# Performance work log

Measured on AMD Instinct MI355X. Metric: run time of the kernel, lower is better.

The kernel has to match this reference:

```python
import jax, jax.numpy as jnp
import numpy as np

B, M, N = 32, 512, 512
XD = YD = 512   # x_size, y_size
S = 512         # shared_size
H = 512         # hidden_size
MAXD = 11       # max relative distance


def _lin(k, i, o):
    lim = float(np.sqrt(6.0 / (i + o)))  # xavier_uniform, gain=1
    return jax.random.uniform(k, (i, o), jnp.float32, -lim, lim)


def setup_inputs() -> dict:
    key = jax.random.key(0)
    ks = jax.random.split(key, 16)
    inp = {
        'prem': jax.random.normal(ks[0], (B, M, YD), jnp.float32),
        'hypo': jax.random.normal(ks[1], (B, N, XD), jnp.float32),
        'prem_mask': jnp.ones((B, M), dtype=bool),
        'hypo_mask': jnp.ones((B, N), dtype=bool),
        # projections
        'Wpx': _lin(ks[2], XD, S), 'bpx': jnp.zeros((S,), jnp.float32),
        'Wpy': _lin(ks[3], YD, S), 'bpy': jnp.zeros((S,), jnp.float32),
        # relative-distance bias embedding (2*max_dist+1, squeezed to scalar)
        'dist_embed': jax.random.normal(ks[4], (2 * MAXD + 1,), jnp.float32),
        # self-attention DeepDot MLP: S -> H -> H
        'Ws1': _lin(ks[5], S, H), 'bs1': jnp.zeros((H,), jnp.float32),
        'Ws2': _lin(ks[6], H, H), 'bs2': jnp.zeros((H,), jnp.float32),
        # cross-attention DeepDot MLP: 2S -> H -> H
        'Wa1': _lin(ks[7], 2 * S, H), 'ba1': jnp.zeros((H,), jnp.float32),
        'Wa2': _lin(ks[8], H, H), 'ba2': jnp.zeros((H,), jnp.float32),
        # compare layer: 4S -> H -> H
        'Wc1': _lin(ks[9], 4 * S, H), 'bc1': jnp.zeros((H,), jnp.float32),
        'Wc2': _lin(ks[10], H, H), 'bc2': jnp.zeros((H,), jnp.float32),
        # aggregate layer: 2H -> H -> H
        'Wg1': _lin(ks[11], 2 * H, H), 'bg1': jnp.zeros((H,), jnp.float32),
        'Wg2': _lin(ks[12], H, H), 'bg2': jnp.zeros((H,), jnp.float32),
    }
    return inp


def _mlp2(x, W1, b1, W2, b2):
    # Linear -> ReLU -> Linear -> ReLU (dropout=0.0)
    h = jax.nn.relu(x @ W1 + b1)
    return jax.nn.relu(h @ W2 + b2)


def _rel_bias(size, dist_embed):
    v = jnp.arange(size)
    d = jnp.clip(v[None, :] - v[:, None], -MAXD, MAXD) + MAXD  # [size,size]
    return dist_embed[d]


def _masked_softmax(t, mask):
    # mask True = valid; broadcast over query dim
    return jax.nn.softmax(jnp.where(mask, t, -jnp.inf), axis=-1)


def reference(prem, hypo, prem_mask, hypo_mask,
              Wpx, bpx, Wpy, bpy, dist_embed,
              Ws1, bs1, Ws2, bs2,
              Wa1, ba1, Wa2, ba2,
              Wc1, bc1, Wc2, bc2,
              Wg1, bg1, Wg2, bg2):
    hypo_p = hypo @ Wpx + bpx   # [B,N,S]
    prem_p = prem @ Wpy + bpy   # [B,M,S]

    # self attention (DeepDot: shared MLP on q and k, then qk^T)
    fp = _mlp2(prem_p, Ws1, bs1, Ws2, bs2)
    fh = _mlp2(hypo_p, Ws1, bs1, Ws2, bs2)
    p_scores = jnp.einsum('bmh,bnh->bmn', fp, fp) + _rel_bias(prem_p.shape[1], dist_embed)[None]
    h_scores = jnp.einsum('bmh,bnh->bmn', fh, fh) + _rel_bias(hypo_p.shape[1], dist_embed)[None]

    p_att = _masked_softmax(p_scores, prem_mask[:, None, :])
    h_att = _masked_softmax(h_scores, hypo_mask[:, None, :])
    prem_ctx = jnp.einsum('bmn,bnd->bmd', p_att, prem_p)
    hypo_ctx = jnp.einsum('bmn,bnd->bmd', h_att, hypo_p)

    prem2 = jnp.concatenate([prem_p, prem_ctx], axis=-1)  # [B,M,2S]
    hypo2 = jnp.concatenate([hypo_p, hypo_ctx], axis=-1)  # [B,N,2S]

    # cross attention
    gp = _mlp2(prem2, Wa1, ba1, Wa2, ba2)
    gh = _mlp2(hypo2, Wa1, ba1, Wa2, ba2)
    sim = jnp.einsum('bmh,bnh->bmn', gp, gh)  # [B,M,N]
    p2h = _masked_softmax(sim, hypo_mask[:, None, :])
    h2p = _masked_softmax(jnp.swapaxes(sim, 1, 2), prem_mask[:, None, :])
    attended_hypo = jnp.einsum('bmn,bnd->bmd', p2h, hypo2)  # [B,M,2S]
    attended_prem = jnp.einsum('bnm,bmd->bnd', h2p, prem2)  # [B,N,2S]

    prem_cmp = _mlp2(jnp.concatenate([prem2, attended_hypo], -1), Wc1, bc1, Wc2, bc2)
    hypo_cmp = _mlp2(jnp.concatenate([hypo2, attended_prem], -1), Wc1, bc1, Wc2, bc2)

    prem_cmp = (prem_cmp * prem_mask[..., None].astype(prem_cmp.dtype)).sum(axis=1)  # [B,H]
    hypo_cmp = (hypo_cmp * hypo_mask[..., None].astype(hypo_cmp.dtype)).sum(axis=1)  # [B,H]

    return _mlp2(jnp.concatenate([prem_cmp, hypo_cmp], -1), Wg1, bg1, Wg2, bg2)
```

## Files before the change

### kernel.cpp

```cpp
#include <hip/hip_runtime.h>
#include <hip/hip_bf16.h>


typedef __bf16 bf16x8 __attribute__((ext_vector_type(8)));
typedef float floatx16 __attribute__((ext_vector_type(16)));

__device__ __forceinline__ unsigned short f32_to_bf16(float f) {
    unsigned int u = __float_as_uint(f);
    unsigned int r = (u + 0x7FFFu + ((u >> 16) & 1u)) >> 16;
    return (unsigned short)r;
}

struct TW {
    const float* src[8];
    unsigned short* dst[8];
    int K[8];
};
__global__ __launch_bounds__(256) void transpose_all_kernel(TW tw) {
    const int z = blockIdx.z;
    const int K = tw.K[z];
    const int k0 = blockIdx.y * 32;
    if (k0 >= K) return;
    const float* W = tw.src[z];
    unsigned short* Wt = tw.dst[z];
    __shared__ unsigned short tile[32][33];
    int n0 = blockIdx.x * 32;
    int tx = threadIdx.x & 31, ty = threadIdx.x >> 5;
    #pragma unroll
    for (int i = 0; i < 4; ++i) {
        int ky = ty + i * 8;
        tile[ky][tx] = f32_to_bf16(W[(long long)(k0 + ky) * 512 + n0 + tx]);
    }
    __syncthreads();
    #pragma unroll
    for (int i = 0; i < 4; ++i) {
        int ny = ty + i * 8;
        Wt[(long long)(n0 + ny) * K + k0 + tx] = tile[tx][ny];
    }
}

template <bool BT, bool AF32>
__global__ __launch_bounds__(256, 4) void gemm_kernel(
    const void* __restrict__ Av, const void* __restrict__ A2v, int lda, long long strideA,
    const unsigned short* __restrict__ Bw, int ldb, long long strideB, int bxor,
    const unsigned short* __restrict__ B2, const float* __restrict__ bias2, int Msplit,
    float* __restrict__ C32, unsigned short* __restrict__ Cb, int ldc, long long strideC,
    const float* __restrict__ bias, int relu, int M, int N, int K,
    float* __restrict__ csum, int swz) {
    constexpr int BBYTES = BT ? 8192 : (32 * 264);
    constexpr int BUF = 8192 + BBYTES;
    __shared__ alignas(16) char smem[2 * BUF];

    const int t = threadIdx.x;
    const int lane = t & 63;
    const int wave = t >> 6;
    const int wm = (wave >> 1) * 64;
    const int wn = (wave & 1) * 64;
    const int ln = lane & 31;
    const int h = lane >> 5;

    int bx = blockIdx.x, by = blockIdx.y;
    if (swz) {
        int Nt = gridDim.x, Mt = gridDim.y;
        int L = by * Nt + bx;
        int x = L & 7, s = L >> 3;
        by = x * (Mt >> 3) + s / Nt;
        bx = s % Nt;
    }
    const int m0 = by * 128;
    const int n0 = bx * 128;
    const int bz = blockIdx.z;
    const int bzB = (bz + bxor) & ((int)gridDim.z - 1);

    const unsigned short* B = Bw;
    const float* biasp = bias;
    long long mA = m0;
    if (Msplit && m0 >= Msplit) {
        if (B2) B = B2;
        if (bias2) biasp = bias2;
        if (A2v) { Av = A2v; mA = m0 - Msplit; }
    }

    const float* aptrF = nullptr;
    const unsigned short* aptrH = nullptr;
    if constexpr (AF32)
        aptrF = (const float*)Av + (long long)bz * strideA +
                (mA + (t >> 1)) * (long long)lda + (t & 1) * 16;
    else
        aptrH = (const unsigned short*)Av + (long long)bz * strideA +
                (mA + (t >> 1)) * (long long)lda + (t & 1) * 16;
    const unsigned short* bptr;
    if (BT)
        bptr = B + (long long)bzB * strideB +
               (long long)(n0 + (t >> 1)) * ldb + (t & 1) * 16;
    else
        bptr = B + (long long)bzB * strideB +
               (long long)(t >> 4) * ldb + n0 + (t & 15) * 8;
    const long long bstep = BT ? 8 : 16 * (long long)ldb;

    const int aoff = ((t & 1) * 256 + (t >> 1)) * 16;
    const int boff = BT ? (8192 + ((t & 1) * 256 + (t >> 1)) * 16)
                        : (8192 + (t >> 4) * 264 + (t & 15) * 16);
    const int boff2 = BT ? 2048 : 16 * 264;

    floatx16 acc[2][2];
    #pragma unroll
    for (int im = 0; im < 2; ++im)
        #pragma unroll
        for (int in = 0; in < 2; ++in)
            acc[im][in] = (floatx16)(0.f);

    uint4 va0, va1, vb0, vb1;
    float4 fa0, fa1, fa2, fa3;

    auto loadA = [&]() {
        if constexpr (AF32) {
            fa0 = *(const float4*)(aptrF);
            fa1 = *(const float4*)(aptrF + 4);
            fa2 = *(const float4*)(aptrF + 8);
            fa3 = *(const float4*)(aptrF + 12);
            aptrF += 32;
        } else {
            va0 = *(const uint4*)(aptrH);
            va1 = *(const uint4*)(aptrH + 8);
            aptrH += 32;
        }
    };
    auto loadB = [&]() {
        vb0 = *(const uint4*)(bptr);
        vb1 = *(const uint4*)(bptr + bstep);
        bptr += BT ? 32 : 32 * (long long)ldb;
    };
    auto commit = [&](char* buf) {
        if constexpr (AF32) {
            union { uint4 q; unsigned short u[8]; } c0, c1;
            c0.u[0] = f32_to_bf16(fa0.x); c0.u[1] = f32_to_bf16(fa0.y);
            c0.u[2] = f32_to_bf16(fa0.z); c0.u[3] = f32_to_bf16(fa0.w);
            c0.u[4] = f32_to_bf16(fa1.x); c0.u[5] = f32_to_bf16(fa1.y);
            c0.u[6] = f32_to_bf16(fa1.z); c0.u[7] = f32_to_bf16(fa1.w);
            c1.u[0] = f32_to_bf16(fa2.x); c1.u[1] = f32_to_bf16(fa2.y);
            c1.u[2] = f32_to_bf16(fa2.z); c1.u[3] = f32_to_bf16(fa2.w);
            c1.u[4] = f32_to_bf16(fa3.x); c1.u[5] = f32_to_bf16(fa3.y);
            c1.u[6] = f32_to_bf16(fa3.z); c1.u[7] = f32_to_bf16(fa3.w);
            *(uint4*)(buf + aoff) = c0.q;
            *(uint4*)(buf + aoff + 2048) = c1.q;
        } else {
            *(uint4*)(buf + aoff) = va0;
            *(uint4*)(buf + aoff + 2048) = va1;
        }
        *(uint4*)(buf + boff) = vb0;
        *(uint4*)(buf + boff + boff2) = vb1;
    };

    loadA(); loadB();
    commit(smem);
    loadA(); loadB();
    __syncthreads();

    int p = 0;
    for (int k0 = 0; k0 < K; k0 += 32) {
        const char* base = smem + p * BUF;
        #pragma unroll
        for (int s = 0; s < 2; ++s) {
            bf16x8 a[2], b[2];
            #pragma unroll
            for (int im = 0; im < 2; ++im)
                a[im] = *(const bf16x8*)(base + ((s * 2 + h) * 128 + wm + im * 32 + ln) * 16);
            if (BT) {
                #pragma unroll
                for (int in = 0; in < 2; ++in)
                    b[in] = *(const bf16x8*)(base + 8192 +
                                             ((s * 2 + h) * 128 + wn + in * 32 + ln) * 16);
            } else {
                #pragma unroll
                for (int in = 0; in < 2; ++in) {
                    union { bf16x8 v; unsigned short u[8]; } u;
                    #pragma unroll
                    for (int j = 0; j < 8; ++j)
                        u.u[j] = *(const unsigned short*)(base + 8192 +
                                 (s * 16 + h * 8 + j) * 264 + (wn + in * 32 + ln) * 2);
                    b[in] = u.v;
                }
            }
            #pragma unroll
            for (int im = 0; im < 2; ++im)
                #pragma unroll
                for (int in = 0; in < 2; ++in)
                    acc[im][in] = __builtin_amdgcn_mfma_f32_32x32x16_bf16(
                        a[im], b[in], acc[im][in], 0, 0, 0);
        }

        if (k0 + 32 < K) {
            commit(smem + (p ^ 1) * BUF);
            if (k0 + 64 < K) { loadA(); loadB(); }
            __syncthreads();
            p ^= 1;
        }
    }

    if (csum) {
        const int bidx = m0 >> 9;
        const long long cbase = (long long)(bidx & 31) * 1024 + (bidx >> 5) * 512;
        #pragma unroll
        for (int in = 0; in < 2; ++in) {
            int n = n0 + wn + in * 32 + ln;
            float bn = biasp ? biasp[n] : 0.f;
            float s = 0.f;
            #pragma unroll
            for (int im = 0; im < 2; ++im)
                #pragma unroll
                for (int r = 0; r < 16; ++r) {
                    float v = acc[im][in][r] + bn;
                    if (relu) v = fmaxf(v, 0.f);
                    s += v;
                }
            s += __shfl_xor(s, 32);
            if (lane < 32) atomicAdd(&csum[cbase + n], s);
        }
        return;
    }

    float* C32b = C32 ? C32 + (long long)bz * strideC : nullptr;
    unsigned short* Cbb = Cb ? Cb + (long long)bz * strideC : nullptr;
    #pragma unroll
    for (int im = 0; im < 2; ++im) {
        #pragma unroll
        for (int in = 0; in < 2; ++in) {
            int n = n0 + wn + in * 32 + ln;
            float bn = biasp ? biasp[n] : 0.f;
            #pragma unroll
            for (int r = 0; r < 16; ++r) {
                int m = m0 + wm + im * 32 + (r & 3) + 8 * (r >> 2) + 4 * h;
                float v = acc[im][in][r] + bn;
                if (relu) v = fmaxf(v, 0.f);
                long long off = (long long)m * ldc + n;
                if (C32b) C32b[off] = v;
                if (Cbb) Cbb[off] = f32_to_bf16(v);
            }
        }
    }
}

__global__ __launch_bounds__(256) void softmax_kernel(const float* S,
                                                      unsigned short* P,
                                                      const float* de, int rel) {
    const int row = blockIdx.x;
    const int b = blockIdx.y;
    const long long baseS = ((long long)b * 512 + row) * 512;
    const long long baseP = ((long long)b * 512 + row) * 1024;
    const int t = threadIdx.x;
    const int lane = t & 63, wv = t >> 6;
    __shared__ float redmax[4], redsum[4];

    float v[2];
    float mx = -1e30f;
    #pragma unroll
    for (int i = 0; i < 2; ++i) {
        int c = t + i * 256;
        float x = S[baseS + c];
        if (rel) {
            int d = c - row;
            d = min(11, max(-11, d));
            x += de[d + 11];
        }
        v[i] = x;
        mx = fmaxf(mx, x);
    }
    #pragma unroll
    for (int o = 32; o > 0; o >>= 1) mx = fmaxf(mx, __shfl_down(mx, o));
    if (lane == 0) redmax[wv] = mx;
    __syncthreads();
    mx = fmaxf(fmaxf(redmax[0], redmax[1]), fmaxf(redmax[2], redmax[3]));

    float s = 0.f;
    #pragma unroll
    for (int i = 0; i < 2; ++i) { v[i] = __expf(v[i] - mx); s += v[i]; }
    #pragma unroll
    for (int o = 32; o > 0; o >>= 1) s += __shfl_down(s, o);
    if (lane == 0) redsum[wv] = s;
    __syncthreads();
    s = redsum[0] + redsum[1] + redsum[2] + redsum[3];
    float inv = 1.f / s;
    #pragma unroll
    for (int i = 0; i < 2; ++i) P[baseP + t + i * 256] = f32_to_bf16(v[i] * inv);
}

__global__ __launch_bounds__(512) void mlp_agg_kernel(const float* __restrict__ X,
                                                      const float* __restrict__ W,
                                                      const float* __restrict__ bias,
                                                      float* __restrict__ out,
                                                      int K, int N, int relu) {
    const int b = blockIdx.y;
    const int nl = threadIdx.x & 63;
    const int n = blockIdx.x * 64 + nl;
    const int ks = threadIdx.x >> 6;
    const int kchunk = K >> 3;
    const float* Xb = X + (long long)b * K;
    const int k0 = ks * kchunk;
    float s = 0.f;
    #pragma unroll 8
    for (int k = k0; k < k0 + kchunk; ++k)
        s += Xb[k] * W[(long long)k * N + n];
    __shared__ float red[8][64];
    red[ks][nl] = s;
    __syncthreads();
    if (threadIdx.x < 64) {
        float t = 0.f;
        #pragma unroll
        for (int i = 0; i < 8; ++i) t += red[i][threadIdx.x];
        t += bias[n];
        if (relu) t = fmaxf(t, 0.f);
        out[(long long)b * N + n] = t;
    }
}

static void gemm(hipStream_t st, bool bt, bool af32,
                 const void* A, const void* A2, int lda, long long sA,
                 const void* B, int ldb, long long sB, int bxor,
                 const void* B2, const float* bias2, int Msplit,
                 float* C32, void* Cb, int ldc, long long sC,
                 const float* bias, int relu, int M, int N, int K, int batch,
                 float* csum = nullptr) {
    dim3 g(N / 128, M / 128, batch), blk(256);
    int swz = (batch == 1 && (M / 128) % 8 == 0) ? 1 : 0;
    if (bt) {
        if (af32)
            gemm_kernel<true, true><<<g, blk, 0, st>>>(
                A, A2, lda, sA, (const unsigned short*)B, ldb, sB, bxor,
                (const unsigned short*)B2, bias2, Msplit,
                C32, (unsigned short*)Cb, ldc, sC, bias, relu, M, N, K, csum, swz);
        else
            gemm_kernel<true, false><<<g, blk, 0, st>>>(
                A, A2, lda, sA, (const unsigned short*)B, ldb, sB, bxor,
                (const unsigned short*)B2, bias2, Msplit,
                C32, (unsigned short*)Cb, ldc, sC, bias, relu, M, N, K, csum, swz);
    } else {
        gemm_kernel<false, false><<<g, blk, 0, st>>>(
            A, A2, lda, sA, (const unsigned short*)B, ldb, sB, bxor,
            (const unsigned short*)B2, bias2, Msplit,
            C32, (unsigned short*)Cb, ldc, sC, bias, relu, M, N, K, csum, swz);
    }
}

extern "C" void kernel_launch(void* const* d_in, const int* in_sizes, int n_in,
                              void* d_out, int out_size, void* d_ws, size_t ws_size,
                              hipStream_t stream) {
    const int B = 32, SEQ = 512;
    const int MT = B * SEQ;
    const int M2 = 2 * MT;

    const float* prem = (const float*)d_in[0];
    const float* hypo = (const float*)d_in[1];
    const float* Wpx = (const float*)d_in[4];  const float* bpx = (const float*)d_in[5];
    const float* Wpy = (const float*)d_in[6];  const float* bpy = (const float*)d_in[7];
    const float* de  = (const float*)d_in[8];
    const float* Ws1 = (const float*)d_in[9];  const float* bs1 = (const float*)d_in[10];
    const float* Ws2 = (const float*)d_in[11]; const float* bs2 = (const float*)d_in[12];
    const float* Wa1 = (const float*)d_in[13]; const float* ba1 = (const float*)d_in[14];
    const float* Wa2 = (const float*)d_in[15]; const float* ba2 = (const float*)d_in[16];
    const float* Wc1 = (const float*)d_in[17]; const float* bc1 = (const float*)d_in[18];
    const float* Wc2 = (const float*)d_in[19]; const float* bc2 = (const float*)d_in[20];
    const float* Wg1 = (const float*)d_in[21]; const float* bg1 = (const float*)d_in[22];
    const float* Wg2 = (const float*)d_in[23]; const float* bg2 = (const float*)d_in[24];

    char* p = (char*)d_ws;
    auto alloc = [&](size_t bytes) { char* r = p; p += (bytes + 255) & ~(size_t)255; return r; };
    unsigned short* prem_bf = (unsigned short*)alloc((size_t)MT * 512 * 2);
    unsigned short* hypo_bf = (unsigned short*)alloc((size_t)MT * 512 * 2);
    unsigned short* premcat = (unsigned short*)alloc((size_t)MT * 2048 * 2);
    unsigned short* hypocat = (unsigned short*)alloc((size_t)MT * 2048 * 2);
    float* scores = (float*)alloc((size_t)64 * SEQ * SEQ * 4);
    unsigned short* h1 = (unsigned short*)scores;
    unsigned short* att = (unsigned short*)scores;
    unsigned short* Wpx_t = (unsigned short*)alloc(512 * 512 * 2);
    unsigned short* Wpy_t = (unsigned short*)alloc(512 * 512 * 2);
    unsigned short* Ws1_t = (unsigned short*)alloc(512 * 512 * 2);
    unsigned short* Ws2_t = (unsigned short*)alloc(512 * 512 * 2);
    unsigned short* Wa1_t = (unsigned short*)alloc(512 * 1024 * 2);
    unsigned short* Wa2_t = (unsigned short*)alloc(512 * 512 * 2);
    unsigned short* Wc1_t = (unsigned short*)alloc(512 * 2048 * 2);
    unsigned short* Wc2_t = (unsigned short*)alloc(512 * 512 * 2);
    float* agg  = (float*)alloc(32 * 1024 * 4);
    float* aggh = (float*)alloc(32 * 512 * 4);
    (void)hypo_bf; (void)hypocat;

    const long long sBM = (long long)SEQ * SEQ;
    const long long sAtt = (long long)SEQ * 1024;
    const long long sCat = (long long)SEQ * 2048;

    {
        TW tw;
        tw.src[0] = Wpy; tw.dst[0] = Wpy_t; tw.K[0] = 512;
        tw.src[1] = Wpx; tw.dst[1] = Wpx_t; tw.K[1] = 512;
        tw.src[2] = Ws1; tw.dst[2] = Ws1_t; tw.K[2] = 512;
        tw.src[3] = Ws2; tw.dst[3] = Ws2_t; tw.K[3] = 512;
        tw.src[4] = Wa1; tw.dst[4] = Wa1_t; tw.K[4] = 1024;
        tw.src[5] = Wa2; tw.dst[5] = Wa2_t; tw.K[5] = 512;
        tw.src[6] = Wc1; tw.dst[6] = Wc1_t; tw.K[6] = 2048;
        tw.src[7] = Wc2; tw.dst[7] = Wc2_t; tw.K[7] = 512;
        transpose_all_kernel<<<dim3(16, 64, 8), 256, 0, stream>>>(tw);
        hipMemsetAsync(agg, 0, 32 * 1024 * sizeof(float), stream);
    }

    gemm(stream, true, true, prem, hypo, 512, 0, Wpy_t, 512, 0, 0,
         Wpx_t, bpx, MT, nullptr, premcat, 2048, 0, bpy, 0, M2, 512, 512, 1);

    gemm(stream, true, false, premcat, nullptr, 2048, 0, Ws1_t, 512, 0, 0,
         nullptr, nullptr, 0, nullptr, h1, 512, 0, bs1, 1, M2, 512, 512, 1);
    gemm(stream, true, false, h1, nullptr, 512, 0, Ws2_t, 512, 0, 0,
         nullptr, nullptr, 0, nullptr, prem_bf, 512, 0, bs2, 1, M2, 512, 512, 1);

    gemm(stream, true, false, prem_bf, nullptr, 512, sBM, prem_bf, 512, sBM, 0,
         nullptr, nullptr, 0, scores, nullptr, 512, sBM, nullptr, 0, 512, 512, 512, 64);
    softmax_kernel<<<dim3(512, 64), 256, 0, stream>>>(scores, att, de, 1);
    gemm(stream, false, false, att, nullptr, 1024, sAtt, premcat, 2048, sCat, 0,
         nullptr, nullptr, 0, nullptr, premcat + 512, 2048, sCat, nullptr, 0, 512, 512, 512, 64);

    gemm(stream, true, false, premcat, nullptr, 2048, 0, Wa1_t, 1024, 0, 0,
         nullptr, nullptr, 0, nullptr, h1, 512, 0, ba1, 1, M2, 512, 1024, 1);
    gemm(stream, true, false, h1, nullptr, 512, 0, Wa2_t, 512, 0, 0,
         nullptr, nullptr, 0, nullptr, prem_bf, 512, 0, ba2, 1, M2, 512, 512, 1);

    gemm(stream, true, false, prem_bf, nullptr, 512, sBM, prem_bf, 512, sBM, 32,
         nullptr, nullptr, 0, scores, nullptr, 512, sBM, nullptr, 0, 512, 512, 512, 64);
    softmax_kernel<<<dim3(512, 64), 256, 0, stream>>>(scores, att, de, 0);
    gemm(stream, false, false, att, nullptr, 1024, sAtt, premcat, 2048, sCat, 32,
         nullptr, nullptr, 0, nullptr, premcat + 1024, 2048, sCat, nullptr, 0, 512, 1024, 512, 64);

    gemm(stream, true, false, premcat, nullptr, 2048, 0, Wc1_t, 2048, 0, 0,
         nullptr, nullptr, 0, nullptr, h1, 512, 0, bc1, 1, M2, 512, 2048, 1);
    gemm(stream, true, false, h1, nullptr, 512, 0, Wc2_t, 512, 0, 0,
         nullptr, nullptr, 0, nullptr, nullptr, 512, 0, bc2, 1, M2, 512, 512, 1, agg);

    mlp_agg_kernel<<<dim3(8, 32), 512, 0, stream>>>(agg, Wg1, bg1, aggh, 1024, 512, 1);
    mlp_agg_kernel<<<dim3(8, 32), 512, 0, stream>>>(aggh, Wg2, bg2, (float*)d_out, 512, 512, 1);
}
```

Baseline: 698.8 us.

## Use direct global-to-LDS loads for bf16 GEMM operands and prefetch before compute

Replaces the register-staged global loads and LDS stores for the bf16 A operand and the transposed B operand with global_load_lds (direct-to-LDS DMA) writes into the double buffer. The next-tile commit and prefetch are moved to the top of the k-loop so they overlap with the MFMA work on the current buffer. This is meant to cut VGPR pressure and the ds_write instructions per tile. The risk is waitcnt handling: the LDS layout written by the DMA must match the reader's indexing, and the vmcnt must drain before the barrier.

```diff
diff --git a/kernel.cpp b/kernel.cpp
--- a/kernel.cpp
+++ b/kernel.cpp
@@ -4,6 +4,11 @@
 
 typedef __bf16 bf16x8 __attribute__((ext_vector_type(8)));
 typedef float floatx16 __attribute__((ext_vector_type(16)));
+
+#define GLOAD16(g, l)                                                          \
+    __builtin_amdgcn_global_load_lds(                                          \
+        (const __attribute__((address_space(1))) void*)(g),                    \
+        (__attribute__((address_space(3))) void*)(l), 16, 0, 0)
 
 __device__ __forceinline__ unsigned short f32_to_bf16(float f) {
     unsigned int u = __float_as_uint(f);
@@ -50,6 +55,7 @@
     constexpr int BBYTES = BT ? 8192 : (32 * 264);
     constexpr int BUF = 8192 + BBYTES;
     __shared__ alignas(16) char smem[2 * BUF];
+    auto s3 = (__attribute__((address_space(3))) char*)smem;
 
     const int t = threadIdx.x;
     const int lane = t & 63;
@@ -82,26 +88,26 @@
     }
 
     const float* aptrF = nullptr;
-    const unsigned short* aptrH = nullptr;
+    const unsigned short* adma = nullptr;
     if constexpr (AF32)
         aptrF = (const float*)Av + (long long)bz * strideA +
                 (mA + (t >> 1)) * (long long)lda + (t & 1) * 16;
     else
-        aptrH = (const unsigned short*)Av + (long long)bz * strideA +
-                (mA + (t >> 1)) * (long long)lda + (t & 1) * 16;
-    const unsigned short* bptr;
-    if (BT)
-        bptr = B + (long long)bzB * strideB +
-               (long long)(n0 + (t >> 1)) * ldb + (t & 1) * 16;
+        adma = (const unsigned short*)Av + (long long)bz * strideA +
+               (mA + (t & 127)) * (long long)lda + (t >> 7) * 8;
+    const unsigned short* bdma = nullptr;
+    const unsigned short* bptr = nullptr;
+    if constexpr (BT)
+        bdma = B + (long long)bzB * strideB +
+               (long long)(n0 + (t & 127)) * ldb + (t >> 7) * 8;
     else
         bptr = B + (long long)bzB * strideB +
                (long long)(t >> 4) * ldb + n0 + (t & 15) * 8;
-    const long long bstep = BT ? 8 : 16 * (long long)ldb;
-
+
+    const int aldsW = (t & ~63) * 16;
     const int aoff = ((t & 1) * 256 + (t >> 1)) * 16;
-    const int boff = BT ? (8192 + ((t & 1) * 256 + (t >> 1)) * 16)
-                        : (8192 + (t >> 4) * 264 + (t & 15) * 16);
-    const int boff2 = BT ? 2048 : 16 * 264;
+    const int boff = 8192 + (t >> 4) * 264 + (t & 15) * 16;
+    constexpr int bstep2 = 16 * 264;
 
     floatx16 acc[2][2];
     #pragma unroll
@@ -110,55 +116,80 @@
         for (int in = 0; in < 2; ++in)
             acc[im][in] = (floatx16)(0.f);
 
-    uint4 va0, va1, vb0, vb1;
+    uint4 vb0, vb1;
     float4 fa0, fa1, fa2, fa3;
-
-    auto loadA = [&]() {
-        if constexpr (AF32) {
-            fa0 = *(const float4*)(aptrF);
-            fa1 = *(const float4*)(aptrF + 4);
-            fa2 = *(const float4*)(aptrF + 8);
-            fa3 = *(const float4*)(aptrF + 12);
-            aptrF += 32;
-        } else {
-            va0 = *(const uint4*)(aptrH);
-            va1 = *(const uint4*)(aptrH + 8);
-            aptrH += 32;
-        }
-    };
-    auto loadB = [&]() {
+    const long long bvstep = 16 * (long long)ldb;
+
+    auto loadA_v = [&]() {
+        fa0 = *(const float4*)(aptrF);
+        fa1 = *(const float4*)(aptrF + 4);
+        fa2 = *(const float4*)(aptrF + 8);
+        fa3 = *(const float4*)(aptrF + 12);
+        aptrF += 32;
+    };
+    auto commitA_v = [&](char* buf) {
+        union { uint4 q; unsigned short u[8]; } c0, c1;
+        c0.u[0] = f32_to_bf16(fa0.x); c0.u[1] = f32_to_bf16(fa0.y);
+        c0.u[2] = f32_to_bf16(fa0.z); c0.u[3] = f32_to_bf16(fa0.w);
+        c0.u[4] = f32_to_bf16(fa1.x); c0.u[5] = f32_to_bf16(fa1.y);
+        c0.u[6] = f32_to_bf16(fa1.z); c0.u[7] = f32_to_bf16(fa1.w);
+        c1.u[0] = f32_to_bf16(fa2.x); c1.u[1] = f32_to_bf16(fa2.y);
+        c1.u[2] = f32_to_bf16(fa2.z); c1.u[3] = f32_to_bf16(fa2.w);
+        c1.u[4] = f32_to_bf16(fa3.x); c1.u[5] = f32_to_bf16(fa3.y);
+        c1.u[6] = f32_to_bf16(fa3.z); c1.u[7] = f32_to_bf16(fa3.w);
+        *(uint4*)(buf + aoff) = c0.q;
+        *(uint4*)(buf + aoff + 2048) = c1.q;
+    };
+    auto loadB_v = [&]() {
         vb0 = *(const uint4*)(bptr);
-        vb1 = *(const uint4*)(bptr + bstep);
-        bptr += BT ? 32 : 32 * (long long)ldb;
-    };
-    auto commit = [&](char* buf) {
-        if constexpr (AF32) {
-            union { uint4 q; unsigned short u[8]; } c0, c1;
-            c0.u[0] = f32_to_bf16(fa0.x); c0.u[1] = f32_to_bf16(fa0.y);
-            c0.u[2] = f32_to_bf16(fa0.z); c0.u[3] = f32_to_bf16(fa0.w);
-            c0.u[4] = f32_to_bf16(fa1.x); c0.u[5] = f32_to_bf16(fa1.y);
-            c0.u[6] = f32_to_bf16(fa1.z); c0.u[7] = f32_to_bf16(fa1.w);
-            c1.u[0] = f32_to_bf16(fa2.x); c1.u[1] = f32_to_bf16(fa2.y);
-            c1.u[2] = f32_to_bf16(fa2.z); c1.u[3] = f32_to_bf16(fa2.w);
-            c1.u[4] = f32_to_bf16(fa3.x); c1.u[5] = f32_to_bf16(fa3.y);
-            c1.u[6] = f32_to_bf16(fa3.z); c1.u[7] = f32_to_bf16(fa3.w);
-            *(uint4*)(buf + aoff) = c0.q;
-            *(uint4*)(buf + aoff + 2048) = c1.q;
-        } else {
-            *(uint4*)(buf + aoff) = va0;
-            *(uint4*)(buf + aoff + 2048) = va1;
-        }
+        vb1 = *(const uint4*)(bptr + bvstep);
+        bptr += 32 * (long long)ldb;
+    };
+    auto commitB_v = [&](char* buf) {
         *(uint4*)(buf + boff) = vb0;
-        *(uint4*)(buf + boff + boff2) = vb1;
-    };
-
-    loadA(); loadB();
-    commit(smem);
-    loadA(); loadB();
+        *(uint4*)(buf + boff + bstep2) = vb1;
+    };
+    auto dmaA = [&](int bufsel) {
+        GLOAD16(adma, s3 + bufsel * BUF + aldsW);
+        GLOAD16(adma + 16, s3 + bufsel * BUF + aldsW + 4096);
+        adma += 32;
+    };
+    auto dmaB = [&](int bufsel) {
+        GLOAD16(bdma, s3 + bufsel * BUF + 8192 + aldsW);
+        GLOAD16(bdma + 16, s3 + bufsel * BUF + 8192 + aldsW + 4096);
+        bdma += 32;
+    };
+
+    if constexpr (AF32) {
+        loadA_v(); commitA_v(smem); loadA_v();
+    } else {
+        dmaA(0);
+    }
+    if constexpr (BT) {
+        dmaB(0);
+    } else {
+        loadB_v(); commitB_v(smem); loadB_v();
+    }
     __syncthreads();
 
     int p = 0;
     for (int k0 = 0; k0 < K; k0 += 32) {
+        if (k0 + 32 < K) {
+            char* nxt = smem + (p ^ 1) * BUF;
+            if constexpr (AF32) {
+                commitA_v(nxt);
+                if (k0 + 64 < K) loadA_v();
+            } else {
+                dmaA(p ^ 1);
+            }
+            if constexpr (BT) {
+                dmaB(p ^ 1);
+            } else {
+                commitB_v(nxt);
+                if (k0 + 64 < K) loadB_v();
+            }
+        }
+
         const char* base = smem + p * BUF;
         #pragma unroll
         for (int s = 0; s < 2; ++s) {
@@ -191,8 +222,6 @@
         }
 
         if (k0 + 32 < K) {
-            commit(smem + (p ^ 1) * BUF);
-            if (k0 + 64 < K) { loadA(); loadB(); }
             __syncthreads();
             p ^= 1;
         }
```

Result: slower. 847.0 us (+21.2%).
